# Kernel tuning notes

Measured on AMD Instinct MI355X. Metric: run time of the kernel, lower is better.

Reference implementation:

```python
import jax, jax.numpy as jnp
import numpy as np

BATCH = 1024
D_IN = 4096
D_OUT = 4096
B = 128  # block size
K_IN = (D_IN + B - 1) // B    # 32
K_OUT = (D_OUT + B - 1) // B  # 32


def setup_inputs() -> dict:
    key = jax.random.key(0)
    kx, kw, kd = jax.random.split(key, 3)
    x = jax.random.normal(kx, (BATCH, D_IN), dtype=jnp.float32)
    W = jax.random.normal(kw, (K_OUT, K_IN, B), dtype=jnp.float32) * 0.1
    # Bernoulli +/-1 diagonal
    D_bernoulli = jnp.where(jax.random.bernoulli(kd, p=0.5, shape=(D_IN,)), 1.0, -1.0).astype(jnp.float32)
    return {"x": x, "W": W, "D_bernoulli": D_bernoulli}


def reference(x, W, D_bernoulli):
    k_out, k_in, b = W.shape
    d_in = D_IN
    d_out = D_OUT
    if x.ndim == 1:
        x = x[None, :]
    batch = x.shape[0]
    # diagonal sign flip
    x_d = x * D_bernoulli[None, :]
    pad_len = k_in * b - d_in
    if pad_len > 0:
        x_d = jnp.pad(x_d, ((0, 0), (0, pad_len)))
    x_blocks = x_d.reshape(batch, k_in, b)
    # frequency-domain block-circulant matmul
    X_fft = jnp.fft.fft(x_blocks, axis=-1)            # (batch, k_in, b) complex
    W_fft = jnp.fft.fft(W, axis=-1)                    # (k_out, k_in, b) complex
    # Y_fft[n,o,:] = sum_j X_fft[n,j,:] * conj(W_fft[o,j,:])
    Y_fft = jnp.einsum('njb,ojb->nob', X_fft, jnp.conjugate(W_fft))
    Y = jnp.fft.ifft(Y_fft, axis=-1).real              # (batch, k_out, b)
    out_flat = Y.reshape(batch, k_out * b)
    if k_out * b > d_out:
        out_flat = out_flat[:, :d_out]
    return out_flat
```

## Files before the change

### kernel.cpp

```cpp
#include <hip/hip_runtime.h>
#include <hip/hip_bf16.h>

#define TWOPI_OVER_B 0.049087385212340517f

typedef __attribute__((ext_vector_type(8))) short bf16x8;
typedef __attribute__((ext_vector_type(4))) float f32x4;

static __device__ __forceinline__ unsigned short f2bf(float f) {
    __hip_bfloat16 h = __float2bfloat16(f);
    return *reinterpret_cast<unsigned short*>(&h);
}
static __device__ __forceinline__ unsigned long long pack4(float a, float b, float c, float d) {
    return (unsigned long long)f2bf(a) | ((unsigned long long)f2bf(b) << 16)
         | ((unsigned long long)f2bf(c) << 32) | ((unsigned long long)f2bf(d) << 48);
}

__global__ __launch_bounds__(256) void k_prep(const float* __restrict__ W,
                                              unsigned short* __restrict__ fragB,
                                              unsigned short* __restrict__ fragCi,
                                              unsigned short* __restrict__ BmatT) {
    __shared__ char smem[73984];
    __shared__ float tbl[256];
    int tid = threadIdx.x;

    if (blockIdx.x < 80) {
        int i = blockIdx.x * 256 + tid;
        if (i < 18432) {
            int e = i & 7, l2 = (i >> 3) & 63, kb = (i >> 9) & 3, c = i >> 11;
            int kr = c * 16 + (l2 & 15);
            int t  = kb * 32 + (l2 >> 4) * 8 + e;
            float v = 0.f;
            if (kr < 65)       v =  cosf(TWOPI_OVER_B * (float)((kr * t) & 127));
            else if (kr < 130) v = -sinf(TWOPI_OVER_B * (float)(((kr - 65) * t) & 127));
            fragB[i] = f2bf(v);
        }
        if (i < 20480) {
            int e = i & 7, l2 = (i >> 3) & 63;
            int ckb = i >> 9; int kb = ckb % 5, c = ckb / 5;
            int kr = kb * 32 + (l2 >> 4) * 8 + e;
            int t  = c * 16 + (l2 & 15);
            float v = 0.f;
            if (kr < 65)       v =  cosf(TWOPI_OVER_B * (float)((kr * t) & 127));
            else if (kr < 130) v = -sinf(TWOPI_OVER_B * (float)(((kr - 65) * t) & 127));
            fragCi[i] = f2bf(v);
        }
        return;
    }

    int bw = blockIdx.x - 80;
    unsigned long long* xs8 = (unsigned long long*)smem;
    float* Yl = (float*)smem;
    unsigned short* fB = (unsigned short*)(smem + 37120);

    for (int i = tid; i < 128; i += 256) {
        float s, c;
        sincosf(TWOPI_OVER_B * (float)i, &s, &c);
        tbl[i] = c; tbl[128 + i] = s;
    }
    __syncthreads();

    for (int i = tid; i < 18432; i += 256) {
        int e = i & 7, l2 = (i >> 3) & 63, kb = (i >> 9) & 3, c = i >> 11;
        int kr = c * 16 + (l2 & 15);
        int t  = kb * 32 + (l2 >> 4) * 8 + e;
        float v = 0.f;
        if (kr < 65)       v =  tbl[(kr * t) & 127];
        else if (kr < 130) v = -tbl[128 + (((kr - 65) * t) & 127)];
        fB[i] = f2bf(v);
    }
    #pragma unroll
    for (int it = 0; it < 8; ++it) {
        int f  = tid + it * 256;
        float4 wa = ((const float4*)W)[(size_t)bw * 2048 + f];
        int rl = f >> 5;
        int t0 = (f & 31) * 4;
        int byte = (rl * 256 + t0 * 2) ^ ((rl & 7) << 4);
        xs8[byte >> 3] = pack4(wa.x, wa.y, wa.z, wa.w);
    }
    __syncthreads();

    int l = tid & 63, w = tid >> 6;
    int rl_a = w * 16 + (l & 15);
    int coff = (l >> 4) * 16;
    bf16x8 a[4];
    #pragma unroll
    for (int kb = 0; kb < 4; ++kb) {
        int byte = (rl_a * 256 + kb * 64 + coff) ^ ((rl_a & 7) << 4);
        a[kb] = *(const bf16x8*)(smem + byte);
    }
    __syncthreads();

    f32x4 acc[9];
    #pragma unroll
    for (int c = 0; c < 9; ++c) acc[c] = (f32x4)0.f;
    #pragma unroll
    for (int c = 0; c < 9; ++c)
        #pragma unroll
        for (int kb = 0; kb < 4; ++kb)
            acc[c] = __builtin_amdgcn_mfma_f32_16x16x32_bf16(a[kb], ((const bf16x8*)fB)[(c * 4 + kb) * 64 + l], acc[c], 0, 0, 0);

    int rowd = w * 16 + (l >> 4) * 4;
    int cold = l & 15;
    #pragma unroll
    for (int c = 0; c < 9; ++c)
        #pragma unroll
        for (int r = 0; r < 4; ++r)
            Yl[(rowd + r) * 145 + c * 16 + cold] = acc[c][r];
    __syncthreads();

    int o0 = bw * 2;
    for (int c2 = tid; c2 < 4160; c2 += 256) {
        int k = c2 >> 6, sub = c2 & 63;
        int oo = sub >> 5, h = (sub >> 4) & 1, t = sub & 15;
        int j0 = t * 4;
        float sc = (k == 0 || k == 64) ? (1.f / 128.f) : (2.f / 128.f);
        int col; float sgn;
        if (j0 < 32) { col = h ? 65 + k : k;  sgn = h ? -sc : sc; }
        else         { col = h ? k : 65 + k;  sgn = sc; }
        int rlb = oo * 32 + (j0 & 31);
        unsigned long long pk = pack4(sgn * Yl[(rlb + 0) * 145 + col], sgn * Yl[(rlb + 1) * 145 + col],
                                      sgn * Yl[(rlb + 2) * 145 + col], sgn * Yl[(rlb + 3) * 145 + col]);
        int o2 = h * 32 + o0 + oo;
        *(unsigned long long*)(BmatT + ((size_t)k * 64 + o2) * 64 + j0) = pk;
    }
}

__global__ __launch_bounds__(256) void k_fdft(const float* __restrict__ x,
                                              const float* __restrict__ D,
                                              const bf16x8* __restrict__ fragB,
                                              unsigned short* __restrict__ Xb) {
    __shared__ char smem[16384];
    unsigned long long* xs8 = (unsigned long long*)smem;
    int tid = threadIdx.x;
    int n0 = blockIdx.x * 2;

    #pragma unroll
    for (int it = 0; it < 8; ++it) {
        int f  = tid + it * 256;
        int nn = f >> 10;
        int f4 = f & 1023;
        float4 xa = ((const float4*)(x + (size_t)(n0 + nn) * 4096))[f4];
        float4 da = ((const float4*)D)[f4];
        int rl = nn * 32 + (f4 >> 5);
        int t0 = (f4 & 31) * 4;
        int byte = (rl * 256 + t0 * 2) ^ ((rl & 7) << 4);
        xs8[byte >> 3] = pack4(xa.x * da.x, xa.y * da.y, xa.z * da.z, xa.w * da.w);
    }
    __syncthreads();

    int l = tid & 63, w = tid >> 6;
    int lr = l & 15, lq = l >> 4;
    int rl_a = w * 16 + lr;
    bf16x8 a[4];
    #pragma unroll
    for (int kb = 0; kb < 4; ++kb) {
        int byte = (rl_a * 256 + kb * 64 + lq * 16) ^ ((rl_a & 7) << 4);
        a[kb] = *(const bf16x8*)(smem + byte);
    }
    f32x4 acc[9];
    #pragma unroll
    for (int c = 0; c < 9; ++c) acc[c] = (f32x4)0.f;
    #pragma unroll
    for (int c = 0; c < 9; ++c)
        #pragma unroll
        for (int kb = 0; kb < 4; ++kb)
            acc[c] = __builtin_amdgcn_mfma_f32_16x16x32_bf16(a[kb], fragB[(c * 4 + kb) * 64 + l], acc[c], 0, 0, 0);

    int rowbase = w * 16 + lq * 4;
    int nn = rowbase >> 5, j0 = rowbase & 31;
    #pragma unroll
    for (int c = 0; c < 9; ++c) {
        int col = c * 16 + lr;
        if (col < 130) {
            int k   = (col < 65) ? col : col - 65;
            int off = (col < 65) ? 0 : 32;
            *(unsigned long long*)(Xb + ((size_t)k * 1024 + n0 + nn) * 64 + off + j0)
                = pack4(acc[c][0], acc[c][1], acc[c][2], acc[c][3]);
        }
    }
}

__global__ __launch_bounds__(256) void k_einsum(const unsigned short* __restrict__ Xb,
                                                const unsigned short* __restrict__ BmatT,
                                                unsigned short* __restrict__ Y2) {
    __shared__ char lds[16384];
    int tid = threadIdx.x, l = tid & 63, w = tid >> 6;
    int k = blockIdx.x >> 3, mt = blockIdx.x & 7;
    int m0 = mt * 128 + w * 32;
    int lr = l & 15, lq = l >> 4;

    bf16x8 a[2][2], b[4][2];
    #pragma unroll
    for (int rf = 0; rf < 2; ++rf)
        #pragma unroll
        for (int kb = 0; kb < 2; ++kb)
            a[rf][kb] = *(const bf16x8*)(Xb + ((size_t)k * 1024 + m0 + rf * 16 + lr) * 64 + kb * 32 + lq * 8);
    #pragma unroll
    for (int cf = 0; cf < 4; ++cf)
        #pragma unroll
        for (int kb = 0; kb < 2; ++kb)
            b[cf][kb] = *(const bf16x8*)(BmatT + ((size_t)k * 64 + cf * 16 + lr) * 64 + kb * 32 + lq * 8);

    f32x4 acc[2][4];
    #pragma unroll
    for (int rf = 0; rf < 2; ++rf)
        #pragma unroll
        for (int cf = 0; cf < 4; ++cf) acc[rf][cf] = (f32x4)0.f;
    #pragma unroll
    for (int rf = 0; rf < 2; ++rf)
        #pragma unroll
        for (int cf = 0; cf < 4; ++cf) {
            acc[rf][cf] = __builtin_amdgcn_mfma_f32_16x16x32_bf16(a[rf][0], b[cf][0], acc[rf][cf], 0, 0, 0);
            acc[rf][cf] = __builtin_amdgcn_mfma_f32_16x16x32_bf16(a[rf][1], b[cf][1], acc[rf][cf], 0, 0, 0);
        }

    #pragma unroll
    for (int rf = 0; rf < 2; ++rf)
        #pragma unroll
        for (int cf = 0; cf < 4; ++cf)
            #pragma unroll
            for (int rr = 0; rr < 4; ++rr) {
                int row = rf * 16 + lq * 4 + rr;
                int col = cf * 16 + lr;
                int byte = w * 4096 + ((row * 128 + col * 2) ^ ((row & 7) << 4));
                *(unsigned short*)(lds + byte) = f2bf(acc[rf][cf][rr]);
            }
    __syncthreads();
    #pragma unroll
    for (int i = 0; i < 4; ++i) {
        int row = i * 8 + (l >> 3);
        int byte = w * 4096 + ((row * 128 + (l & 7) * 16) ^ ((row & 7) << 4));
        bf16x8 v = *(const bf16x8*)(lds + byte);
        *(bf16x8*)(Y2 + ((size_t)k * 1024 + m0 + row) * 64 + (l & 7) * 8) = v;
    }
}

__global__ __launch_bounds__(256) void k_idft(const unsigned short* __restrict__ Y2,
                                              const bf16x8* __restrict__ fragCi,
                                              float* __restrict__ out) {
    __shared__ char smem[20480];
    int tid = threadIdx.x;
    int row0 = blockIdx.x * 64;
    int n0 = blockIdx.x * 2;

    for (int i = tid; i < 1920; i += 256) {
        int rl = i / 30, cp = 130 + i % 30;
        int byte = (rl * 320 + cp * 2) ^ ((rl & 7) << 4);
        *(unsigned short*)(smem + byte) = 0;
    }
    for (int c2 = tid; c2 < 2080; c2 += 256) {
        int k = c2 >> 5, sub = c2 & 31, nn = sub >> 4, t = sub & 15;
        unsigned long long v = *(const unsigned long long*)(Y2 + ((size_t)k * 1024 + n0 + nn) * 64 + t * 4);
        int o2_0 = t * 4;
        int col = (o2_0 < 32) ? k : 65 + k;
        int r0 = nn * 32 + (o2_0 & 31);
        #pragma unroll
        for (int i = 0; i < 4; ++i) {
            int rl = r0 + i;
            int byte = (rl * 320 + col * 2) ^ ((rl & 7) << 4);
            *(unsigned short*)(smem + byte) = (unsigned short)(v >> (16 * i));
        }
    }
    __syncthreads();

    int l = tid & 63, w = tid >> 6;
    int rl_a = w * 16 + (l & 15);
    int coff = (l >> 4) * 16;
    bf16x8 a[5];
    #pragma unroll
    for (int kb = 0; kb < 5; ++kb) {
        int byte = (rl_a * 320 + kb * 64 + coff) ^ ((rl_a & 7) << 4);
        a[kb] = *(const bf16x8*)(smem + byte);
    }
    f32x4 acc[8];
    #pragma unroll
    for (int c = 0; c < 8; ++c) acc[c] = (f32x4)0.f;
    #pragma unroll
    for (int c = 0; c < 8; ++c)
        #pragma unroll
        for (int kb = 0; kb < 5; ++kb)
            acc[c] = __builtin_amdgcn_mfma_f32_16x16x32_bf16(a[kb], fragCi[(c * 5 + kb) * 64 + l], acc[c], 0, 0, 0);

    int rowd = row0 + w * 16 + (l >> 4) * 4;
    int cold = l & 15;
    #pragma unroll
    for (int c = 0; c < 8; ++c)
        #pragma unroll
        for (int r = 0; r < 4; ++r)
            out[(size_t)(rowd + r) * 128 + c * 16 + cold] = acc[c][r];
}

extern "C" void kernel_launch(void* const* d_in, const int* in_sizes, int n_in,
                              void* d_out, int out_size, void* d_ws, size_t ws_size,
                              hipStream_t stream) {
    const float* x = (const float*)d_in[0];
    const float* W = (const float*)d_in[1];
    const float* D = (const float*)d_in[2];
    float* out = (float*)d_out;
    float* ws  = (float*)d_ws;

    unsigned short* BmatT  = (unsigned short*)ws;
    unsigned short* Xb     = (unsigned short*)(ws + 133120);
    unsigned short* Y2     = (unsigned short*)(ws + 2263040);
    unsigned short* fragB  = (unsigned short*)(ws + 4392960);
    unsigned short* fragCi = fragB + 18432;

    k_prep  <<<96, 256, 0, stream>>>(W, fragB, fragCi, BmatT);
    k_fdft  <<<512, 256, 0, stream>>>(x, D, (const bf16x8*)fragB, Xb);
    k_einsum<<<520, 256, 0, stream>>>(Xb, BmatT, Y2);
    k_idft  <<<512, 256, 0, stream>>>(Y2, (const bf16x8*)fragCi, out);
}
```

Measured before the change: 49.70 us.

## Halve per-block work in DFT/einsum kernels and fold twiddle generation into weight prep

Forward DFT, einsum and inverse DFT kernels now process one batch row (or 64 rows) per block with 2x2 wave splits, doubling grid sizes to raise occupancy across CUs. The forward DFT loads x directly into registers instead of staging through LDS, then transposes through an LDS tile for coalesced Xb writes. The twiddle fragment tables are now built by the 16 weight-prep blocks from a shared sin/cos table rather than by 80 extra blocks calling cosf/sinf. This trades more blocks and some redundant fragment loads for better latency hiding.

```diff
diff --git a/kernel.cpp b/kernel.cpp
--- a/kernel.cpp
+++ b/kernel.cpp
@@ -20,42 +20,17 @@
                                               unsigned short* __restrict__ fragCi,
                                               unsigned short* __restrict__ BmatT) {
     __shared__ char smem[73984];
+    __shared__ unsigned short fB[18432];
     __shared__ float tbl[256];
     int tid = threadIdx.x;
-
-    if (blockIdx.x < 80) {
-        int i = blockIdx.x * 256 + tid;
-        if (i < 18432) {
-            int e = i & 7, l2 = (i >> 3) & 63, kb = (i >> 9) & 3, c = i >> 11;
-            int kr = c * 16 + (l2 & 15);
-            int t  = kb * 32 + (l2 >> 4) * 8 + e;
-            float v = 0.f;
-            if (kr < 65)       v =  cosf(TWOPI_OVER_B * (float)((kr * t) & 127));
-            else if (kr < 130) v = -sinf(TWOPI_OVER_B * (float)(((kr - 65) * t) & 127));
-            fragB[i] = f2bf(v);
-        }
-        if (i < 20480) {
-            int e = i & 7, l2 = (i >> 3) & 63;
-            int ckb = i >> 9; int kb = ckb % 5, c = ckb / 5;
-            int kr = kb * 32 + (l2 >> 4) * 8 + e;
-            int t  = c * 16 + (l2 & 15);
-            float v = 0.f;
-            if (kr < 65)       v =  cosf(TWOPI_OVER_B * (float)((kr * t) & 127));
-            else if (kr < 130) v = -sinf(TWOPI_OVER_B * (float)(((kr - 65) * t) & 127));
-            fragCi[i] = f2bf(v);
-        }
-        return;
-    }
-
-    int bw = blockIdx.x - 80;
+    int bw = blockIdx.x;
     unsigned long long* xs8 = (unsigned long long*)smem;
     float* Yl = (float*)smem;
-    unsigned short* fB = (unsigned short*)(smem + 37120);
-
-    for (int i = tid; i < 128; i += 256) {
+
+    if (tid < 128) {
         float s, c;
-        sincosf(TWOPI_OVER_B * (float)i, &s, &c);
-        tbl[i] = c; tbl[128 + i] = s;
+        sincosf(TWOPI_OVER_B * (float)tid, &s, &c);
+        tbl[tid] = c; tbl[128 + tid] = s;
     }
     __syncthreads();
 
@@ -67,6 +42,25 @@
         if (kr < 65)       v =  tbl[(kr * t) & 127];
         else if (kr < 130) v = -tbl[128 + (((kr - 65) * t) & 127)];
         fB[i] = f2bf(v);
+    }
+    for (int i = bw * 1152 + tid; i < (bw + 1) * 1152; i += 256) {
+        int e = i & 7, l2 = (i >> 3) & 63, kb = (i >> 9) & 3, c = i >> 11;
+        int kr = c * 16 + (l2 & 15);
+        int t  = kb * 32 + (l2 >> 4) * 8 + e;
+        float v = 0.f;
+        if (kr < 65)       v =  tbl[(kr * t) & 127];
+        else if (kr < 130) v = -tbl[128 + (((kr - 65) * t) & 127)];
+        fragB[i] = f2bf(v);
+    }
+    for (int i = bw * 1280 + tid; i < (bw + 1) * 1280; i += 256) {
+        int e = i & 7, l2 = (i >> 3) & 63;
+        int ckb = i >> 9; int kb = ckb % 5, c = ckb / 5;
+        int kr = kb * 32 + (l2 >> 4) * 8 + e;
+        int t  = c * 16 + (l2 & 15);
+        float v = 0.f;
+        if (kr < 65)       v =  tbl[(kr * t) & 127];
+        else if (kr < 130) v = -tbl[128 + (((kr - 65) * t) & 127)];
+        fragCi[i] = f2bf(v);
     }
     #pragma unroll
     for (int it = 0; it < 8; ++it) {
@@ -129,107 +123,105 @@
                                               const float* __restrict__ D,
                                               const bf16x8* __restrict__ fragB,
                                               unsigned short* __restrict__ Xb) {
-    __shared__ char smem[16384];
-    unsigned long long* xs8 = (unsigned long long*)smem;
-    int tid = threadIdx.x;
-    int n0 = blockIdx.x * 2;
-
-    #pragma unroll
-    for (int it = 0; it < 8; ++it) {
-        int f  = tid + it * 256;
-        int nn = f >> 10;
-        int f4 = f & 1023;
-        float4 xa = ((const float4*)(x + (size_t)(n0 + nn) * 4096))[f4];
-        float4 da = ((const float4*)D)[f4];
-        int rl = nn * 32 + (f4 >> 5);
-        int t0 = (f4 & 31) * 4;
-        int byte = (rl * 256 + t0 * 2) ^ ((rl & 7) << 4);
-        xs8[byte >> 3] = pack4(xa.x * da.x, xa.y * da.y, xa.z * da.z, xa.w * da.w);
-    }
-    __syncthreads();
-
-    int l = tid & 63, w = tid >> 6;
+    __shared__ float Yl[32 * 145];
+    int tid = threadIdx.x, l = tid & 63, w = tid >> 6;
     int lr = l & 15, lq = l >> 4;
-    int rl_a = w * 16 + lr;
-    bf16x8 a[4];
+    int wr = w & 1, wc = w >> 1;
+    int n = blockIdx.x;
+
+    int j = wr * 16 + lr;
+    const float* xr = x + (size_t)n * 4096 + j * 128 + lq * 8;
+    const float* Dr = D + j * 128 + lq * 8;
+    union { bf16x8 v; unsigned long long q[2]; } au[4];
     #pragma unroll
     for (int kb = 0; kb < 4; ++kb) {
-        int byte = (rl_a * 256 + kb * 64 + lq * 16) ^ ((rl_a & 7) << 4);
-        a[kb] = *(const bf16x8*)(smem + byte);
-    }
-    f32x4 acc[9];
-    #pragma unroll
-    for (int c = 0; c < 9; ++c) acc[c] = (f32x4)0.f;
-    #pragma unroll
-    for (int c = 0; c < 9; ++c)
-        #pragma unroll
-        for (int kb = 0; kb < 4; ++kb)
-            acc[c] = __builtin_amdgcn_mfma_f32_16x16x32_bf16(a[kb], fragB[(c * 4 + kb) * 64 + l], acc[c], 0, 0, 0);
-
-    int rowbase = w * 16 + lq * 4;
-    int nn = rowbase >> 5, j0 = rowbase & 31;
-    #pragma unroll
-    for (int c = 0; c < 9; ++c) {
-        int col = c * 16 + lr;
-        if (col < 130) {
-            int k   = (col < 65) ? col : col - 65;
-            int off = (col < 65) ? 0 : 32;
-            *(unsigned long long*)(Xb + ((size_t)k * 1024 + n0 + nn) * 64 + off + j0)
-                = pack4(acc[c][0], acc[c][1], acc[c][2], acc[c][3]);
-        }
+        float4 x0 = *(const float4*)(xr + kb * 32);
+        float4 x1 = *(const float4*)(xr + kb * 32 + 4);
+        float4 d0 = *(const float4*)(Dr + kb * 32);
+        float4 d1 = *(const float4*)(Dr + kb * 32 + 4);
+        au[kb].q[0] = pack4(x0.x * d0.x, x0.y * d0.y, x0.z * d0.z, x0.w * d0.w);
+        au[kb].q[1] = pack4(x1.x * d1.x, x1.y * d1.y, x1.z * d1.z, x1.w * d1.w);
+    }
+
+    int cbase = wc * 5;
+    f32x4 acc[5];
+    #pragma unroll
+    for (int ci = 0; ci < 5; ++ci) acc[ci] = (f32x4)0.f;
+    #pragma unroll
+    for (int ci = 0; ci < 5; ++ci) {
+        int c = cbase + ci;
+        if (c < 9) {
+            #pragma unroll
+            for (int kb = 0; kb < 4; ++kb)
+                acc[ci] = __builtin_amdgcn_mfma_f32_16x16x32_bf16(au[kb].v, fragB[(c * 4 + kb) * 64 + l], acc[ci], 0, 0, 0);
+        }
+    }
+
+    int rowd = wr * 16 + lq * 4;
+    #pragma unroll
+    for (int ci = 0; ci < 5; ++ci) {
+        int c = cbase + ci;
+        if (c < 9) {
+            #pragma unroll
+            for (int r = 0; r < 4; ++r)
+                Yl[(rowd + r) * 145 + c * 16 + lr] = acc[ci][r];
+        }
+    }
+    __syncthreads();
+
+    for (int c2 = tid; c2 < 1040; c2 += 256) {
+        int k = c2 >> 4, t = c2 & 15;
+        int j0 = t * 4;
+        int col = (j0 < 32) ? k : 65 + k;
+        int rlb = j0 & 31;
+        unsigned long long pk = pack4(Yl[(rlb + 0) * 145 + col], Yl[(rlb + 1) * 145 + col],
+                                      Yl[(rlb + 2) * 145 + col], Yl[(rlb + 3) * 145 + col]);
+        *(unsigned long long*)(Xb + ((size_t)k * 1024 + n) * 64 + j0) = pk;
     }
 }
 
 __global__ __launch_bounds__(256) void k_einsum(const unsigned short* __restrict__ Xb,
                                                 const unsigned short* __restrict__ BmatT,
                                                 unsigned short* __restrict__ Y2) {
-    __shared__ char lds[16384];
+    __shared__ char lds[8192];
     int tid = threadIdx.x, l = tid & 63, w = tid >> 6;
-    int k = blockIdx.x >> 3, mt = blockIdx.x & 7;
-    int m0 = mt * 128 + w * 32;
+    int k = blockIdx.x >> 4, mt = blockIdx.x & 15;
+    int m0 = mt * 64 + w * 16;
     int lr = l & 15, lq = l >> 4;
 
-    bf16x8 a[2][2], b[4][2];
-    #pragma unroll
-    for (int rf = 0; rf < 2; ++rf)
-        #pragma unroll
-        for (int kb = 0; kb < 2; ++kb)
-            a[rf][kb] = *(const bf16x8*)(Xb + ((size_t)k * 1024 + m0 + rf * 16 + lr) * 64 + kb * 32 + lq * 8);
+    bf16x8 a[2], b[4][2];
+    #pragma unroll
+    for (int kb = 0; kb < 2; ++kb)
+        a[kb] = *(const bf16x8*)(Xb + ((size_t)k * 1024 + m0 + lr) * 64 + kb * 32 + lq * 8);
     #pragma unroll
     for (int cf = 0; cf < 4; ++cf)
         #pragma unroll
         for (int kb = 0; kb < 2; ++kb)
             b[cf][kb] = *(const bf16x8*)(BmatT + ((size_t)k * 64 + cf * 16 + lr) * 64 + kb * 32 + lq * 8);
 
-    f32x4 acc[2][4];
-    #pragma unroll
-    for (int rf = 0; rf < 2; ++rf)
-        #pragma unroll
-        for (int cf = 0; cf < 4; ++cf) acc[rf][cf] = (f32x4)0.f;
-    #pragma unroll
-    for (int rf = 0; rf < 2; ++rf)
-        #pragma unroll
-        for (int cf = 0; cf < 4; ++cf) {
-            acc[rf][cf] = __builtin_amdgcn_mfma_f32_16x16x32_bf16(a[rf][0], b[cf][0], acc[rf][cf], 0, 0, 0);
-            acc[rf][cf] = __builtin_amdgcn_mfma_f32_16x16x32_bf16(a[rf][1], b[cf][1], acc[rf][cf], 0, 0, 0);
-        }
-
-    #pragma unroll
-    for (int rf = 0; rf < 2; ++rf)
-        #pragma unroll
-        for (int cf = 0; cf < 4; ++cf)
-            #pragma unroll
-            for (int rr = 0; rr < 4; ++rr) {
-                int row = rf * 16 + lq * 4 + rr;
-                int col = cf * 16 + lr;
-                int byte = w * 4096 + ((row * 128 + col * 2) ^ ((row & 7) << 4));
-                *(unsigned short*)(lds + byte) = f2bf(acc[rf][cf][rr]);
-            }
-    __syncthreads();
-    #pragma unroll
-    for (int i = 0; i < 4; ++i) {
+    f32x4 acc[4];
+    #pragma unroll
+    for (int cf = 0; cf < 4; ++cf) acc[cf] = (f32x4)0.f;
+    #pragma unroll
+    for (int cf = 0; cf < 4; ++cf) {
+        acc[cf] = __builtin_amdgcn_mfma_f32_16x16x32_bf16(a[0], b[cf][0], acc[cf], 0, 0, 0);
+        acc[cf] = __builtin_amdgcn_mfma_f32_16x16x32_bf16(a[1], b[cf][1], acc[cf], 0, 0, 0);
+    }
+
+    #pragma unroll
+    for (int cf = 0; cf < 4; ++cf)
+        #pragma unroll
+        for (int rr = 0; rr < 4; ++rr) {
+            int row = lq * 4 + rr;
+            int col = cf * 16 + lr;
+            int byte = w * 2048 + ((row * 128 + col * 2) ^ ((row & 7) << 4));
+            *(unsigned short*)(lds + byte) = f2bf(acc[cf][rr]);
+        }
+    __syncthreads();
+    #pragma unroll
+    for (int i = 0; i < 2; ++i) {
         int row = i * 8 + (l >> 3);
-        int byte = w * 4096 + ((row * 128 + (l & 7) * 16) ^ ((row & 7) << 4));
+        int byte = w * 2048 + ((row * 128 + (l & 7) * 16) ^ ((row & 7) << 4));
         bf16x8 v = *(const bf16x8*)(lds + byte);
         *(bf16x8*)(Y2 + ((size_t)k * 1024 + m0 + row) * 64 + (l & 7) * 8) = v;
     }
@@ -238,22 +230,23 @@
 __global__ __launch_bounds__(256) void k_idft(const unsigned short* __restrict__ Y2,
                                               const bf16x8* __restrict__ fragCi,
                                               float* __restrict__ out) {
-    __shared__ char smem[20480];
+    __shared__ char smem[10240];
     int tid = threadIdx.x;
-    int row0 = blockIdx.x * 64;
-    int n0 = blockIdx.x * 2;
-
-    for (int i = tid; i < 1920; i += 256) {
-        int rl = i / 30, cp = 130 + i % 30;
-        int byte = (rl * 320 + cp * 2) ^ ((rl & 7) << 4);
-        *(unsigned short*)(smem + byte) = 0;
-    }
-    for (int c2 = tid; c2 < 2080; c2 += 256) {
-        int k = c2 >> 5, sub = c2 & 31, nn = sub >> 4, t = sub & 15;
-        unsigned long long v = *(const unsigned long long*)(Y2 + ((size_t)k * 1024 + n0 + nn) * 64 + t * 4);
+    int n = blockIdx.x;
+
+    for (int i = tid; i < 1024; i += 256) {
+        int rl = i >> 5, cc = i & 31;
+        if (cc < 30) {
+            int byte = (rl * 320 + (130 + cc) * 2) ^ ((rl & 7) << 4);
+            *(unsigned short*)(smem + byte) = 0;
+        }
+    }
+    for (int c2 = tid; c2 < 1040; c2 += 256) {
+        int k = c2 >> 4, t = c2 & 15;
+        unsigned long long v = *(const unsigned long long*)(Y2 + ((size_t)k * 1024 + n) * 64 + t * 4);
         int o2_0 = t * 4;
         int col = (o2_0 < 32) ? k : 65 + k;
-        int r0 = nn * 32 + (o2_0 & 31);
+        int r0 = o2_0 & 31;
         #pragma unroll
         for (int i = 0; i < 4; ++i) {
             int rl = r0 + i;
@@ -264,30 +257,31 @@
     __syncthreads();
 
     int l = tid & 63, w = tid >> 6;
-    int rl_a = w * 16 + (l & 15);
-    int coff = (l >> 4) * 16;
+    int lr = l & 15, lq = l >> 4;
+    int wr = w & 1, wc = w >> 1;
+    int rl_a = wr * 16 + lr;
     bf16x8 a[5];
     #pragma unroll
     for (int kb = 0; kb < 5; ++kb) {
-        int byte = (rl_a * 320 + kb * 64 + coff) ^ ((rl_a & 7) << 4);
+        int byte = (rl_a * 320 + kb * 64 + lq * 16) ^ ((rl_a & 7) << 4);
         a[kb] = *(const bf16x8*)(smem + byte);
     }
-    f32x4 acc[8];
-    #pragma unroll
-    for (int c = 0; c < 8; ++c) acc[c] = (f32x4)0.f;
-    #pragma unroll
-    for (int c = 0; c < 8; ++c)
+    int cbase = wc * 4;
+    f32x4 acc[4];
+    #pragma unroll
+    for (int ci = 0; ci < 4; ++ci) acc[ci] = (f32x4)0.f;
+    #pragma unroll
+    for (int ci = 0; ci < 4; ++ci)
         #pragma unroll
         for (int kb = 0; kb < 5; ++kb)
-            acc[c] = __builtin_amdgcn_mfma_f32_16x16x32_bf16(a[kb], fragCi[(c * 5 + kb) * 64 + l], acc[c], 0, 0, 0);
-
-    int rowd = row0 + w * 16 + (l >> 4) * 4;
-    int cold = l & 15;
-    #pragma unroll
-    for (int c = 0; c < 8; ++c)
+            acc[ci] = __builtin_amdgcn_mfma_f32_16x16x32_bf16(a[kb], fragCi[((cbase + ci) * 5 + kb) * 64 + l], acc[ci], 0, 0, 0);
+
+    int rowg = n * 32 + wr * 16 + lq * 4;
+    #pragma unroll
+    for (int ci = 0; ci < 4; ++ci)
         #pragma unroll
         for (int r = 0; r < 4; ++r)
-            out[(size_t)(rowd + r) * 128 + c * 16 + cold] = acc[c][r];
+            out[(size_t)(rowg + r) * 128 + (cbase + ci) * 16 + lr] = acc[ci][r];
 }
 
 extern "C" void kernel_launch(void* const* d_in, const int* in_sizes, int n_in,
@@ -305,8 +299,8 @@
     unsigned short* fragB  = (unsigned short*)(ws + 4392960);
     unsigned short* fragCi = fragB + 18432;
 
-    k_prep  <<<96, 256, 0, stream>>>(W, fragB, fragCi, BmatT);
-    k_fdft  <<<512, 256, 0, stream>>>(x, D, (const bf16x8*)fragB, Xb);
-    k_einsum<<<520, 256, 0, stream>>>(Xb, BmatT, Y2);
-    k_idft  <<<512, 256, 0, stream>>>(Y2, (const bf16x8*)fragCi, out);
-}
+    k_prep  <<<16,   256, 0, stream>>>(W, fragB, fragCi, BmatT);
+    k_fdft  <<<1024, 256, 0, stream>>>(x, D, (const bf16x8*)fragB, Xb);
+    k_einsum<<<1040, 256, 0, stream>>>(Xb, BmatT, Y2);
+    k_idft  <<<1024, 256, 0, stream>>>(Y2, (const bf16x8*)fragCi, out);
+}
```

Result: slower. 51.39 us (+3.4%).

## Fold DFT table generation into W-prep blocks and stage fdft output through LDS

Applied to the files above, without the earlier changes.

The 80 dedicated blocks that computed fragB/fragCi with cosf/sinf are removed. The 16 W-prep blocks now each write a slice of those tables from a shared-memory sincos lookup table, so k_prep launches 16 blocks instead of 96. k_fdft now writes its MFMA accumulators to an LDS tile and repacks them so each 8-byte global store writes along the contiguous j dimension, which is meant to coalesce the Xb writes. The cost is extra LDS traffic, two more barriers and a larger LDS footprint in k_fdft, which may lower occupancy.

```diff
diff --git a/kernel.cpp b/kernel.cpp
--- a/kernel.cpp
+++ b/kernel.cpp
@@ -20,42 +20,17 @@
                                               unsigned short* __restrict__ fragCi,
                                               unsigned short* __restrict__ BmatT) {
     __shared__ char smem[73984];
+    __shared__ unsigned short fB[18432];
     __shared__ float tbl[256];
     int tid = threadIdx.x;
-
-    if (blockIdx.x < 80) {
-        int i = blockIdx.x * 256 + tid;
-        if (i < 18432) {
-            int e = i & 7, l2 = (i >> 3) & 63, kb = (i >> 9) & 3, c = i >> 11;
-            int kr = c * 16 + (l2 & 15);
-            int t  = kb * 32 + (l2 >> 4) * 8 + e;
-            float v = 0.f;
-            if (kr < 65)       v =  cosf(TWOPI_OVER_B * (float)((kr * t) & 127));
-            else if (kr < 130) v = -sinf(TWOPI_OVER_B * (float)(((kr - 65) * t) & 127));
-            fragB[i] = f2bf(v);
-        }
-        if (i < 20480) {
-            int e = i & 7, l2 = (i >> 3) & 63;
-            int ckb = i >> 9; int kb = ckb % 5, c = ckb / 5;
-            int kr = kb * 32 + (l2 >> 4) * 8 + e;
-            int t  = c * 16 + (l2 & 15);
-            float v = 0.f;
-            if (kr < 65)       v =  cosf(TWOPI_OVER_B * (float)((kr * t) & 127));
-            else if (kr < 130) v = -sinf(TWOPI_OVER_B * (float)(((kr - 65) * t) & 127));
-            fragCi[i] = f2bf(v);
-        }
-        return;
-    }
-
-    int bw = blockIdx.x - 80;
+    int bw = blockIdx.x;
     unsigned long long* xs8 = (unsigned long long*)smem;
     float* Yl = (float*)smem;
-    unsigned short* fB = (unsigned short*)(smem + 37120);
-
-    for (int i = tid; i < 128; i += 256) {
+
+    if (tid < 128) {
         float s, c;
-        sincosf(TWOPI_OVER_B * (float)i, &s, &c);
-        tbl[i] = c; tbl[128 + i] = s;
+        sincosf(TWOPI_OVER_B * (float)tid, &s, &c);
+        tbl[tid] = c; tbl[128 + tid] = s;
     }
     __syncthreads();
 
@@ -67,6 +42,25 @@
         if (kr < 65)       v =  tbl[(kr * t) & 127];
         else if (kr < 130) v = -tbl[128 + (((kr - 65) * t) & 127)];
         fB[i] = f2bf(v);
+    }
+    for (int i = bw * 1152 + tid; i < (bw + 1) * 1152; i += 256) {
+        int e = i & 7, l2 = (i >> 3) & 63, kb = (i >> 9) & 3, c = i >> 11;
+        int kr = c * 16 + (l2 & 15);
+        int t  = kb * 32 + (l2 >> 4) * 8 + e;
+        float v = 0.f;
+        if (kr < 65)       v =  tbl[(kr * t) & 127];
+        else if (kr < 130) v = -tbl[128 + (((kr - 65) * t) & 127)];
+        fragB[i] = f2bf(v);
+    }
+    for (int i = bw * 1280 + tid; i < (bw + 1) * 1280; i += 256) {
+        int e = i & 7, l2 = (i >> 3) & 63;
+        int ckb = i >> 9; int kb = ckb % 5, c = ckb / 5;
+        int kr = kb * 32 + (l2 >> 4) * 8 + e;
+        int t  = c * 16 + (l2 & 15);
+        float v = 0.f;
+        if (kr < 65)       v =  tbl[(kr * t) & 127];
+        else if (kr < 130) v = -tbl[128 + (((kr - 65) * t) & 127)];
+        fragCi[i] = f2bf(v);
     }
     #pragma unroll
     for (int it = 0; it < 8; ++it) {
@@ -129,8 +123,9 @@
                                               const float* __restrict__ D,
                                               const bf16x8* __restrict__ fragB,
                                               unsigned short* __restrict__ Xb) {
-    __shared__ char smem[16384];
+    __shared__ char smem[37120];
     unsigned long long* xs8 = (unsigned long long*)smem;
+    float* Yl = (float*)smem;
     int tid = threadIdx.x;
     int n0 = blockIdx.x * 2;
 
@@ -149,12 +144,12 @@
     __syncthreads();
 
     int l = tid & 63, w = tid >> 6;
-    int lr = l & 15, lq = l >> 4;
-    int rl_a = w * 16 + lr;
+    int rl_a = w * 16 + (l & 15);
+    int coff = (l >> 4) * 16;
     bf16x8 a[4];
     #pragma unroll
     for (int kb = 0; kb < 4; ++kb) {
-        int byte = (rl_a * 256 + kb * 64 + lq * 16) ^ ((rl_a & 7) << 4);
+        int byte = (rl_a * 256 + kb * 64 + coff) ^ ((rl_a & 7) << 4);
         a[kb] = *(const bf16x8*)(smem + byte);
     }
     f32x4 acc[9];
@@ -165,18 +160,25 @@
         #pragma unroll
         for (int kb = 0; kb < 4; ++kb)
             acc[c] = __builtin_amdgcn_mfma_f32_16x16x32_bf16(a[kb], fragB[(c * 4 + kb) * 64 + l], acc[c], 0, 0, 0);
-
-    int rowbase = w * 16 + lq * 4;
-    int nn = rowbase >> 5, j0 = rowbase & 31;
-    #pragma unroll
-    for (int c = 0; c < 9; ++c) {
-        int col = c * 16 + lr;
-        if (col < 130) {
-            int k   = (col < 65) ? col : col - 65;
-            int off = (col < 65) ? 0 : 32;
-            *(unsigned long long*)(Xb + ((size_t)k * 1024 + n0 + nn) * 64 + off + j0)
-                = pack4(acc[c][0], acc[c][1], acc[c][2], acc[c][3]);
-        }
+    __syncthreads();
+
+    int rowd = w * 16 + (l >> 4) * 4;
+    int cold = l & 15;
+    #pragma unroll
+    for (int c = 0; c < 9; ++c)
+        #pragma unroll
+        for (int r = 0; r < 4; ++r)
+            Yl[(rowd + r) * 145 + c * 16 + cold] = acc[c][r];
+    __syncthreads();
+
+    for (int c2 = tid; c2 < 2080; c2 += 256) {
+        int k = c2 >> 5, sub = c2 & 31, nn = sub >> 4, t = sub & 15;
+        int j0 = t * 4;
+        int col = (j0 < 32) ? k : 65 + k;
+        int rlb = nn * 32 + (j0 & 31);
+        unsigned long long pk = pack4(Yl[(rlb + 0) * 145 + col], Yl[(rlb + 1) * 145 + col],
+                                      Yl[(rlb + 2) * 145 + col], Yl[(rlb + 3) * 145 + col]);
+        *(unsigned long long*)(Xb + ((size_t)k * 1024 + n0 + nn) * 64 + j0) = pk;
     }
 }
 
@@ -305,7 +307,7 @@
     unsigned short* fragB  = (unsigned short*)(ws + 4392960);
     unsigned short* fragCi = fragB + 18432;
 
-    k_prep  <<<96, 256, 0, stream>>>(W, fragB, fragCi, BmatT);
+    k_prep  <<<16,  256, 0, stream>>>(W, fragB, fragCi, BmatT);
     k_fdft  <<<512, 256, 0, stream>>>(x, D, (const bf16x8*)fragB, Xb);
     k_einsum<<<520, 256, 0, stream>>>(Xb, BmatT, Y2);
     k_idft  <<<512, 256, 0, stream>>>(Y2, (const bf16x8*)fragCi, out);
```

After: 49.86 us. Within noise of the previous version (+0.3%).
